# Optimization experiments

Hardware: AMD Instinct MI355X
Metric: run time of the kernel (lower is better)

The kernel has to match this reference:

```python
import jax, jax.numpy as jnp
import numpy as np

D = 2048           # model dim
E = 8              # num experts
K = 2              # top_k
H = int(D * 8 / 3) # SwiGLU hidden dim (5461), matches torch default
B, S = 2, 2048


def setup_inputs() -> dict:
    key = jax.random.key(0)
    ks = jax.random.split(key, 5)
    x = jax.random.normal(ks[0], (B, S, D), jnp.float32)
    wg = jax.random.normal(ks[1], (E, D), jnp.float32) * 0.02   # gate Linear weight [out,in]
    w1 = jax.random.normal(ks[2], (E, H, D), jnp.float32) * 0.02  # per-expert w1 [H,D]
    w2 = jax.random.normal(ks[3], (E, D, H), jnp.float32) * 0.02  # per-expert w2 [D,H]
    w3 = jax.random.normal(ks[4], (E, H, D), jnp.float32) * 0.02  # per-expert w3 [H,D]
    return {"x": x, "wg": wg, "w1": w1, "w2": w2, "w3": w3}


def reference(x, wg, w1, w2, w3):
    b, s, d = x.shape
    xf = x.reshape(-1, d)                         # [T, D]
    T = xf.shape[0]

    # --- gating (eval mode: no noise) ---
    logits = xf @ wg.T                            # [T, E]
    topk_vals, topk_idx = jax.lax.top_k(logits, K)  # [T, K]
    topk_probs = jax.nn.softmax(topk_vals, axis=-1)  # softmax over the K selected
    gate_probs = jax.nn.softmax(logits, axis=-1)     # [T, E] for load-balancing loss
    mean_probs = gate_probs.mean(axis=0)             # [E]
    # torch .std() is unbiased (ddof=1)
    lb_loss = (jnp.std(mean_probs, ddof=1) / (mean_probs.mean() + 1e-10)) ** 2

    # --- combine weights: scatter top-k probs into dense [T, E] ---
    cw = jnp.zeros((T, E), xf.dtype).at[jnp.arange(T)[:, None], topk_idx].add(topk_probs)

    # --- per-expert SwiGLU over all tokens (dense grouped GEMMs) ---
    h = jax.nn.silu(jnp.einsum('td,ehd->eth', xf, w1)) * jnp.einsum('td,ehd->eth', xf, w3)
    ye = jnp.einsum('eth,edh->etd', h, w2)        # [E, T, D]

    # --- weighted combine ---
    out = jnp.einsum('etd,te->td', ye, cw).reshape(b, s, d)
    return out, 0.01 * lb_loss
```

## Files before the change

kernel.cpp:

```cpp
#include <hip/hip_runtime.h>
#include <hip/hip_bf16.h>

#define Tn 4096
#define Dm 2048
#define En 8
#define Hh 5461
#define HP 5504

typedef __attribute__((ext_vector_type(8))) short bf16x8;
typedef __attribute__((ext_vector_type(4))) float f32x4;

__device__ __forceinline__ unsigned short f2bf(float f) {
  union { __hip_bfloat16 b; unsigned short u; } c;
  c.b = __float2bfloat16(f);
  return c.u;
}

__device__ __forceinline__ uint4 pack8(const float* f) {
  union { unsigned short us[8]; uint4 v; } o;
#pragma unroll
  for (int i = 0; i < 8; ++i) o.us[i] = f2bf(f[i]);
  return o.v;
}

__device__ __forceinline__ void gl16(const void* g, void* lds) {
  __builtin_amdgcn_global_load_lds(
      (const __attribute__((address_space(1))) unsigned int*)g,
      (__attribute__((address_space(3))) unsigned int*)lds, 16, 0, 0);
}

#define WAIT6_BAR() asm volatile("s_waitcnt vmcnt(6)\n\ts_barrier" ::: "memory")
#define WAIT4_BAR() asm volatile("s_waitcnt vmcnt(4)\n\ts_barrier" ::: "memory")
#define WAIT0_BAR() asm volatile("s_waitcnt vmcnt(0)\n\ts_barrier" ::: "memory")
#define LGK0_BAR()  asm volatile("s_waitcnt lgkmcnt(0)\n\ts_barrier" ::: "memory")


__global__ __launch_bounds__(64) void gating_kernel(
    const float* __restrict__ x, const float* __restrict__ wg,
    float* __restrict__ gate_p, int* __restrict__ topk_e, float* __restrict__ topk_p,
    unsigned short* __restrict__ xb)
{
  const int t = blockIdx.x;
  const int l = threadIdx.x;
  const float* xr = x + (size_t)t * Dm;
  float acc[En];
#pragma unroll
  for (int e = 0; e < En; ++e) acc[e] = 0.f;
  for (int d = l; d < Dm; d += 64) {
    const float xv = xr[d];
#pragma unroll
    for (int e = 0; e < En; ++e) acc[e] = fmaf(xv, wg[e * Dm + d], acc[e]);
  }
#pragma unroll
  for (int e = 0; e < En; ++e) {
    float v = acc[e];
#pragma unroll
    for (int s = 32; s > 0; s >>= 1) v += __shfl_xor(v, s);
    acc[e] = v;
  }
  unsigned short* xrow = xb + (size_t)t * Dm;
#pragma unroll
  for (int k = 0; k < 4; ++k) {
    const int b = k * 512 + l * 8;
    float f[8];
    *(float4*)(f)     = *(const float4*)(xr + b);
    *(float4*)(f + 4) = *(const float4*)(xr + b + 4);
    *(uint4*)(xrow + b) = pack8(f);
  }
  if (l == 0) {
    float m = acc[0];
    for (int e = 1; e < En; ++e) m = fmaxf(m, acc[e]);
    float p[En]; float s = 0.f;
    for (int e = 0; e < En; ++e) { p[e] = __expf(acc[e] - m); s += p[e]; }
    const float inv = 1.f / s;
    for (int e = 0; e < En; ++e) gate_p[t * En + e] = p[e] * inv;
    int e0 = 0; float v0 = acc[0];
    for (int e = 1; e < En; ++e) if (acc[e] > v0) { v0 = acc[e]; e0 = e; }
    int e1 = -1; float v1 = -3.4e38f;
    for (int e = 0; e < En; ++e) if (e != e0 && acc[e] > v1) { v1 = acc[e]; e1 = e; }
    const float q  = __expf(v1 - v0);
    const float q0 = 1.f / (1.f + q);
    const float q1 = q * q0;
    topk_e[t * 2] = e0; topk_e[t * 2 + 1] = e1;
    topk_p[t * 2] = q0; topk_p[t * 2 + 1] = q1;
  }
}

__global__ __launch_bounds__(256) void reduce_scatter_kernel(
    const int* __restrict__ topk_e, const float* __restrict__ topk_p,
    const float* __restrict__ gate_p,
    int* __restrict__ counts, int* __restrict__ offs,
    int* __restrict__ pair_token, float* __restrict__ pair_w,
    float* __restrict__ out_scalar)
{
  __shared__ int cnt_s[En];
  __shared__ int run_s[En];
  __shared__ float red[256 * En];
  const int tid = threadIdx.x;
  if (tid < En) cnt_s[tid] = 0;
  __syncthreads();
  for (int i = tid; i < Tn * 2; i += 256) atomicAdd(&cnt_s[topk_e[i]], 1);
  __syncthreads();
  if (tid == 0) {
    int o = 0;
    for (int e = 0; e < En; ++e) {
      offs[e] = o; run_s[e] = o; counts[e] = cnt_s[e]; o += cnt_s[e];
    }
  }
  __syncthreads();
  for (int i = tid; i < Tn * 2; i += 256) {
    const int e = topk_e[i];
    const int slot = atomicAdd(&run_s[e], 1);
    pair_token[slot] = i >> 1;
    pair_w[slot] = topk_p[i];
  }
  float p8[En];
#pragma unroll
  for (int e = 0; e < En; ++e) p8[e] = 0.f;
  for (int t = tid; t < Tn; t += 256)
#pragma unroll
    for (int e = 0; e < En; ++e) p8[e] += gate_p[t * En + e];
#pragma unroll
  for (int e = 0; e < En; ++e) red[tid * En + e] = p8[e];
  __syncthreads();
  for (int s = 128; s > 0; s >>= 1) {
    if (tid < s)
#pragma unroll
      for (int e = 0; e < En; ++e) red[tid * En + e] += red[(tid + s) * En + e];
    __syncthreads();
  }
  if (tid == 0) {
    double mp[En]; double sum = 0.0;
    for (int e = 0; e < En; ++e) { mp[e] = (double)red[e] / (double)Tn; sum += mp[e]; }
    const double mean = sum / En;
    double var = 0.0;
    for (int e = 0; e < En; ++e) { const double d = mp[e] - mean; var += d * d; }
    var /= (En - 1);
    const double denom = mean + 1e-10;
    *out_scalar = (float)(0.01 * var / (denom * denom));
  }
}

__global__ __launch_bounds__(256) void cvt_w13_kernel(
    const float* __restrict__ w1, const float* __restrict__ w3,
    unsigned short* __restrict__ w1b, unsigned short* __restrict__ w3b)
{
  const float* src = blockIdx.y ? w3 : w1;
  unsigned short* dst = blockIdx.y ? w3b : w1b;
  const unsigned i = ((unsigned)blockIdx.x * 256u + threadIdx.x) * 8u;
  const unsigned per_e = (unsigned)HP * Dm;
  const unsigned e = i / per_e;
  const unsigned r = i % per_e;
  const unsigned row = r / Dm, col = r % Dm;
  uint4 v;
  if (row < Hh) {
    const float* s = src + (size_t)e * Hh * Dm + (size_t)row * Dm + col;
    float f[8];
    *(float4*)(f)     = *(const float4*)(s);
    *(float4*)(f + 4) = *(const float4*)(s + 4);
    v = pack8(f);
  } else {
    v = (uint4){0, 0, 0, 0};
  }
  *(uint4*)(dst + i) = v;
}

__global__ __launch_bounds__(256) void cvt_w2_kernel(const float* __restrict__ w2,
                                                     unsigned short* __restrict__ w2b)
{
  const unsigned i = ((unsigned)blockIdx.x * 256u + threadIdx.x) * 8u;
  const unsigned per_e = (unsigned)Dm * HP;
  const unsigned e = i / per_e;
  const unsigned r = i % per_e;
  const unsigned row = r / HP, col = r % HP;
  const float* s = w2 + (size_t)e * Dm * Hh + (size_t)row * Hh + col;
  float f[8];
#pragma unroll
  for (int k = 0; k < 8; ++k) f[k] = (col + k < Hh) ? s[k] : 0.f;
  *(uint4*)(w2b + i) = pack8(f);
}

__global__ __launch_bounds__(256, 2) void gemm1_kernel(
    const unsigned short* __restrict__ xb,
    const unsigned short* __restrict__ w1b, const unsigned short* __restrict__ w3b,
    const int* __restrict__ counts, const int* __restrict__ offs,
    const int* __restrict__ pair_token,
    unsigned short* __restrict__ h)
{
  const int bid = blockIdx.x;
  const int logical = (bid & 7) * 344 + (bid >> 3);
  const int z  = logical & 7;
  const int pe = logical >> 3;
  const int e  = pe & 7;
  const int jp = pe >> 3;

  const int cnt = counts[e];
  if (cnt <= 0) return;
  const int base = offs[e];
  const int j0 = jp * 128;
  const int tid = threadIdx.x;
  const int l = tid & 63;
  const int wid = tid >> 6;
  const int wr = wid >> 1, wc = wid & 1;

  __shared__ unsigned short As[2][128 * 32];
  __shared__ unsigned short B1[2][128 * 32];
  __shared__ unsigned short B3[2][128 * 32];

  const int r0 = tid >> 2;
  const int r1 = 64 + (tid >> 2);
  const int c0 = (((tid & 3) ^ ((tid >> 3) & 3))) * 8;
  const int wb0 = wid * 512;
  const int wb1 = 2048 + wid * 512;

  const unsigned short* b1r0 = w1b + ((size_t)e * HP + j0 + r0) * Dm + c0;
  const unsigned short* b1r1 = w1b + ((size_t)e * HP + j0 + r1) * Dm + c0;
  const unsigned short* b3r0 = w3b + ((size_t)e * HP + j0 + r0) * Dm + c0;
  const unsigned short* b3r1 = w3b + ((size_t)e * HP + j0 + r1) * Dm + c0;

  const int lr = l & 15;
  const int sq = (((l >> 4) ^ ((lr >> 1) & 3))) * 8;

#define STAGE1(b, kk) do { \
    gl16(a0 + (kk), &As[b][wb0]);   gl16(a1 + (kk), &As[b][wb1]); \
    gl16(b1r0 + (kk), &B1[b][wb0]); gl16(b1r1 + (kk), &B1[b][wb1]); \
    gl16(b3r0 + (kk), &B3[b][wb0]); gl16(b3r1 + (kk), &B3[b][wb1]); \
  } while (0)

#define COMPUTE1(b) do { \
    bf16x8 av[4], b1v[4], b3v[4]; \
    _Pragma("unroll") \
    for (int m = 0; m < 4; ++m) \
      av[m] = *(const bf16x8*)(&As[b][(wr * 64 + m * 16 + lr) * 32 + sq]); \
    _Pragma("unroll") \
    for (int n = 0; n < 4; ++n) { \
      b1v[n] = *(const bf16x8*)(&B1[b][(wc * 64 + n * 16 + lr) * 32 + sq]); \
      b3v[n] = *(const bf16x8*)(&B3[b][(wc * 64 + n * 16 + lr) * 32 + sq]); \
    } \
    _Pragma("unroll") \
    for (int m = 0; m < 4; ++m) \
      _Pragma("unroll") \
      for (int n = 0; n < 4; ++n) { \
        acc1[m][n] = __builtin_amdgcn_mfma_f32_16x16x32_bf16(av[m], b1v[n], acc1[m][n], 0, 0, 0); \
        acc3[m][n] = __builtin_amdgcn_mfma_f32_16x16x32_bf16(av[m], b3v[n], acc3[m][n], 0, 0, 0); \
      } \
  } while (0)

  for (int mt = z; mt * 128 < cnt; mt += 8) {
    const int row0 = mt * 128;
    int s0 = row0 + r0; if (s0 >= cnt) s0 = cnt - 1;
    int s1 = row0 + r1; if (s1 >= cnt) s1 = cnt - 1;
    const unsigned short* a0 = xb + (size_t)pair_token[base + s0] * Dm + c0;
    const unsigned short* a1 = xb + (size_t)pair_token[base + s1] * Dm + c0;

    f32x4 acc1[4][4], acc3[4][4];
#pragma unroll
    for (int m = 0; m < 4; ++m)
#pragma unroll
      for (int n = 0; n < 4; ++n) {
        acc1[m][n] = (f32x4){0.f, 0.f, 0.f, 0.f};
        acc3[m][n] = (f32x4){0.f, 0.f, 0.f, 0.f};
      }

    STAGE1(0, 0);
    int cur = 0;
    for (int kk = 0; kk < Dm - 32; kk += 32) {
      STAGE1(cur ^ 1, kk + 32);
      WAIT6_BAR();
      COMPUTE1(cur);
      LGK0_BAR();
      cur ^= 1;
    }
    WAIT0_BAR();
    COMPUTE1(cur);
    LGK0_BAR();

#pragma unroll
    for (int m = 0; m < 4; ++m) {
      const int rb = wr * 64 + m * 16 + ((l >> 4) << 2);
#pragma unroll
      for (int i = 0; i < 4; ++i) {
        const int sl2 = row0 + rb + i;
        if (sl2 < cnt) {
          unsigned short* hrow = h + (size_t)(base + sl2) * HP + j0 + wc * 64 + lr;
#pragma unroll
          for (int n = 0; n < 4; ++n) {
            const float aa = acc1[m][n][i];
            const float g = aa / (1.f + __expf(-aa));
            hrow[n * 16] = f2bf(g * acc3[m][n][i]);
          }
        }
      }
    }
  }
#undef STAGE1
#undef COMPUTE1
}

__global__ __launch_bounds__(256, 2) void gemm2_kernel(
    const unsigned short* __restrict__ h, const unsigned short* __restrict__ w2b,
    const int* __restrict__ counts, const int* __restrict__ offs,
    const int* __restrict__ pair_token, const float* __restrict__ pair_w,
    float* __restrict__ out)
{
  const int bid = blockIdx.x;
  const int logical = (bid & 7) * 128 + (bid >> 3);
  const int z  = logical & 7;
  const int pe = logical >> 3;
  const int e  = pe & 7;
  const int dp = pe >> 3;

  const int cnt = counts[e];
  if (cnt <= 0) return;
  const int base = offs[e];
  const int d0 = dp * 128;
  const int tid = threadIdx.x;
  const int l = tid & 63;
  const int wid = tid >> 6;
  const int wr = wid >> 1, wc = wid & 1;

  __shared__ unsigned short Ah[2][128 * 32];
  __shared__ unsigned short Bs[2][128 * 32];

  const int r0 = tid >> 2;
  const int r1 = 64 + (tid >> 2);
  const int c0 = (((tid & 3) ^ ((tid >> 3) & 3))) * 8;
  const int wb0 = wid * 512;
  const int wb1 = 2048 + wid * 512;

  const unsigned short* br0 = w2b + ((size_t)e * Dm + d0 + r0) * HP + c0;
  const unsigned short* br1 = w2b + ((size_t)e * Dm + d0 + r1) * HP + c0;

  const int lr = l & 15;
  const int sq = (((l >> 4) ^ ((lr >> 1) & 3))) * 8;

#define STAGE2(b, kk) do { \
    gl16(a0 + (kk), &Ah[b][wb0]); gl16(a1 + (kk), &Ah[b][wb1]); \
    gl16(br0 + (kk), &Bs[b][wb0]); gl16(br1 + (kk), &Bs[b][wb1]); \
  } while (0)

#define COMPUTE2(b) do { \
    bf16x8 av[4], bv[4]; \
    _Pragma("unroll") \
    for (int m = 0; m < 4; ++m) \
      av[m] = *(const bf16x8*)(&Ah[b][(wr * 64 + m * 16 + lr) * 32 + sq]); \
    _Pragma("unroll") \
    for (int n = 0; n < 4; ++n) \
      bv[n] = *(const bf16x8*)(&Bs[b][(wc * 64 + n * 16 + lr) * 32 + sq]); \
    _Pragma("unroll") \
    for (int m = 0; m < 4; ++m) \
      _Pragma("unroll") \
      for (int n = 0; n < 4; ++n) \
        acc[m][n] = __builtin_amdgcn_mfma_f32_16x16x32_bf16(av[m], bv[n], acc[m][n], 0, 0, 0); \
  } while (0)

  for (int mt = z; mt * 128 < cnt; mt += 8) {
    const int row0 = mt * 128;
    int s0 = row0 + r0; if (s0 >= cnt) s0 = cnt - 1;
    int s1 = row0 + r1; if (s1 >= cnt) s1 = cnt - 1;
    const unsigned short* a0 = h + (size_t)(base + s0) * HP + c0;
    const unsigned short* a1 = h + (size_t)(base + s1) * HP + c0;

    f32x4 acc[4][4];
#pragma unroll
    for (int m = 0; m < 4; ++m)
#pragma unroll
      for (int n = 0; n < 4; ++n) acc[m][n] = (f32x4){0.f, 0.f, 0.f, 0.f};

    STAGE2(0, 0);
    int cur = 0;
    for (int kk = 0; kk < HP - 32; kk += 32) {
      STAGE2(cur ^ 1, kk + 32);
      WAIT4_BAR();
      COMPUTE2(cur);
      LGK0_BAR();
      cur ^= 1;
    }
    WAIT0_BAR();
    COMPUTE2(cur);
    LGK0_BAR();

#pragma unroll
    for (int m = 0; m < 4; ++m) {
      const int rb = row0 + wr * 64 + m * 16 + ((l >> 4) << 2);
#pragma unroll
      for (int i = 0; i < 4; ++i) {
        const int sl2 = rb + i;
        if (sl2 < cnt) {
          const int s2 = base + sl2;
          const float pw = pair_w[s2];
          float* orow = out + (size_t)pair_token[s2] * Dm + d0 + wc * 64 + lr;
#pragma unroll
          for (int n = 0; n < 4; ++n)
            atomicAdd(&orow[n * 16], acc[m][n][i] * pw);
        }
      }
    }
  }
#undef STAGE2
#undef COMPUTE2
}

extern "C" void kernel_launch(void* const* d_in, const int* in_sizes, int n_in,
                              void* d_out, int out_size, void* d_ws, size_t ws_size,
                              hipStream_t stream) {
  const float* x  = (const float*)d_in[0];
  const float* wg = (const float*)d_in[1];
  const float* w1 = (const float*)d_in[2];
  const float* w2 = (const float*)d_in[3];
  const float* w3 = (const float*)d_in[4];
  float* out = (float*)d_out;

  char* ws = (char*)d_ws;
  int*    counts     = (int*)(ws + 64);
  int*    offs       = (int*)(ws + 128);
  int*    topk_e     = (int*)(ws + 1024);
  float*  topk_p     = (float*)(ws + 40960);
  int*    pair_token = (int*)(ws + 81920);
  float*  pair_w     = (float*)(ws + 122880);
  float*  gate_p     = (float*)(ws + 163840);
  const size_t MB = 1u << 20;
  unsigned short* xb  = (unsigned short*)(ws + 1 * MB);
  unsigned short* h   = (unsigned short*)(ws + 17 * MB);
  unsigned short* w1b = (unsigned short*)(ws + 104 * MB);
  unsigned short* w3b = (unsigned short*)(ws + 276 * MB);
  unsigned short* w2b = (unsigned short*)(ws + 448 * MB);

  hipMemsetAsync(d_out, 0, (size_t)out_size * sizeof(float), stream);

  gating_kernel  <<<Tn, 64, 0, stream>>>(x, wg, gate_p, topk_e, topk_p, xb);
  reduce_scatter_kernel<<<1, 256, 0, stream>>>(topk_e, topk_p, gate_p, counts, offs,
                                               pair_token, pair_w, out + (size_t)Tn * Dm);
  cvt_w13_kernel <<<dim3(En * HP * Dm / 8 / 256, 2), 256, 0, stream>>>(w1, w3, w1b, w3b);
  cvt_w2_kernel  <<<En * Dm * HP / 8 / 256, 256, 0, stream>>>(w2, w2b);
  gemm1_kernel   <<<43 * En * 8, 256, 0, stream>>>(xb, w1b, w3b, counts, offs, pair_token, h);
  gemm2_kernel   <<<(Dm / 128) * En * 8, 256, 0, stream>>>(h, w2b, counts, offs, pair_token, pair_w, out);
}
```

Before: 1.505 ms.

## Replace atomic scatter-add in gemm2 with per-slot stores and a combine kernel

gemm2 now writes each expert output row to a dense per-slot buffer (reusing the w1b region after gemm1 finishes) instead of weighting and atomically adding into the output. A new combine kernel gathers each token's two expert rows by slot index and forms the weighted sum, which removes the output memset and the float atomics. gemm2's launch bounds also change to ask for 3 blocks per SM. The cost is an extra write and read of an 8192x2048 fp32 intermediate and one more kernel launch, and the higher occupancy target may squeeze registers in gemm2.

New measurement: 1.483 ms. No clear change (-1.5%).

```diff
diff --git a/kernel.cpp b/kernel.cpp
--- a/kernel.cpp
+++ b/kernel.cpp
@@ -90,7 +90,7 @@
     const int* __restrict__ topk_e, const float* __restrict__ topk_p,
     const float* __restrict__ gate_p,
     int* __restrict__ counts, int* __restrict__ offs,
-    int* __restrict__ pair_token, float* __restrict__ pair_w,
+    int* __restrict__ pair_token, int* __restrict__ slot_of,
     float* __restrict__ out_scalar)
 {
   __shared__ int cnt_s[En];
@@ -112,7 +112,7 @@
     const int e = topk_e[i];
     const int slot = atomicAdd(&run_s[e], 1);
     pair_token[slot] = i >> 1;
-    pair_w[slot] = topk_p[i];
+    slot_of[i] = slot;
   }
   float p8[En];
 #pragma unroll
@@ -297,11 +297,10 @@
 #undef COMPUTE1
 }
 
-__global__ __launch_bounds__(256, 2) void gemm2_kernel(
+__global__ __launch_bounds__(256, 3) void gemm2_kernel(
     const unsigned short* __restrict__ h, const unsigned short* __restrict__ w2b,
     const int* __restrict__ counts, const int* __restrict__ offs,
-    const int* __restrict__ pair_token, const float* __restrict__ pair_w,
-    float* __restrict__ out)
+    float* __restrict__ y)
 {
   const int bid = blockIdx.x;
   const int logical = (bid & 7) * 128 + (bid >> 3);
@@ -387,18 +386,40 @@
       for (int i = 0; i < 4; ++i) {
         const int sl2 = rb + i;
         if (sl2 < cnt) {
-          const int s2 = base + sl2;
-          const float pw = pair_w[s2];
-          float* orow = out + (size_t)pair_token[s2] * Dm + d0 + wc * 64 + lr;
+          float* yrow = y + (size_t)(base + sl2) * Dm + d0 + wc * 64 + lr;
 #pragma unroll
           for (int n = 0; n < 4; ++n)
-            atomicAdd(&orow[n * 16], acc[m][n][i] * pw);
+            yrow[n * 16] = acc[m][n][i];
         }
       }
     }
   }
 #undef STAGE2
 #undef COMPUTE2
+}
+
+__global__ __launch_bounds__(256) void combine_kernel(
+    const float* __restrict__ y, const int* __restrict__ slot_of,
+    const float* __restrict__ topk_p, float* __restrict__ out)
+{
+  const int t = blockIdx.x;
+  const int s0 = slot_of[t * 2], s1 = slot_of[t * 2 + 1];
+  const float w0 = topk_p[t * 2], w1 = topk_p[t * 2 + 1];
+  const float* y0 = y + (size_t)s0 * Dm;
+  const float* y1 = y + (size_t)s1 * Dm;
+  float* o = out + (size_t)t * Dm;
+  const int c = threadIdx.x * 8;
+  float4 a0 = *(const float4*)(y0 + c);
+  float4 a1 = *(const float4*)(y0 + c + 4);
+  float4 b0 = *(const float4*)(y1 + c);
+  float4 b1 = *(const float4*)(y1 + c + 4);
+  float4 r0, r1;
+  r0.x = w0 * a0.x + w1 * b0.x; r0.y = w0 * a0.y + w1 * b0.y;
+  r0.z = w0 * a0.z + w1 * b0.z; r0.w = w0 * a0.w + w1 * b0.w;
+  r1.x = w0 * a1.x + w1 * b1.x; r1.y = w0 * a1.y + w1 * b1.y;
+  r1.z = w0 * a1.z + w1 * b1.z; r1.w = w0 * a1.w + w1 * b1.w;
+  *(float4*)(o + c) = r0;
+  *(float4*)(o + c + 4) = r1;
 }
 
 extern "C" void kernel_launch(void* const* d_in, const int* in_sizes, int n_in,
@@ -417,22 +438,22 @@
   int*    topk_e     = (int*)(ws + 1024);
   float*  topk_p     = (float*)(ws + 40960);
   int*    pair_token = (int*)(ws + 81920);
-  float*  pair_w     = (float*)(ws + 122880);
   float*  gate_p     = (float*)(ws + 163840);
+  int*    slot_of    = (int*)(ws + 307200);
   const size_t MB = 1u << 20;
   unsigned short* xb  = (unsigned short*)(ws + 1 * MB);
   unsigned short* h   = (unsigned short*)(ws + 17 * MB);
   unsigned short* w1b = (unsigned short*)(ws + 104 * MB);
   unsigned short* w3b = (unsigned short*)(ws + 276 * MB);
   unsigned short* w2b = (unsigned short*)(ws + 448 * MB);
-
-  hipMemsetAsync(d_out, 0, (size_t)out_size * sizeof(float), stream);
+  float* y = (float*)(ws + 104 * MB);
 
   gating_kernel  <<<Tn, 64, 0, stream>>>(x, wg, gate_p, topk_e, topk_p, xb);
   reduce_scatter_kernel<<<1, 256, 0, stream>>>(topk_e, topk_p, gate_p, counts, offs,
-                                               pair_token, pair_w, out + (size_t)Tn * Dm);
+                                               pair_token, slot_of, out + (size_t)Tn * Dm);
   cvt_w13_kernel <<<dim3(En * HP * Dm / 8 / 256, 2), 256, 0, stream>>>(w1, w3, w1b, w3b);
   cvt_w2_kernel  <<<En * Dm * HP / 8 / 256, 256, 0, stream>>>(w2, w2b);
   gemm1_kernel   <<<43 * En * 8, 256, 0, stream>>>(xb, w1b, w3b, counts, offs, pair_token, h);
-  gemm2_kernel   <<<(Dm / 128) * En * 8, 256, 0, stream>>>(h, w2b, counts, offs, pair_token, pair_w, out);
-}
+  gemm2_kernel   <<<(Dm / 128) * En * 8, 256, 0, stream>>>(h, w2b, counts, offs, y);
+  combine_kernel <<<Tn, 256, 0, stream>>>(y, slot_of, topk_p, out);
+}
```
